# Optimization experiments

Hardware: AMD Instinct MI355X
Metric: run time of the kernel (lower is better)

The kernel has to match this reference:

```python
import jax, jax.numpy as jnp
import numpy as np

HID = 10
IN_DIM = 256
B, H, W = 8, 96, 96


def _conv(x, w, b=None, pad=0):
    y = jax.lax.conv_general_dilated(x, w, (1, 1), [(pad, pad), (pad, pad)],
                                     dimension_numbers=('NCHW', 'OIHW', 'NCHW'))
    return y if b is None else y + b[None, :, None, None]


def _bn(x, g, b):
    # eval-mode InPlaceABN(Sync) with identity running stats -> per-channel affine
    return x * g[None, :, None, None] + b[None, :, None, None]


def _branch(x, w1, g1, b1, w2, g2, b2):
    # Conv3x3 -> BN -> ReLU -> Conv1x1 -> BN -> ReLU  (relation / comp_u / comp_l)
    y = jax.nn.relu(_bn(_conv(x, w1, pad=1), g1, b1))
    return jax.nn.relu(_bn(_conv(y, w2), g2, b2))


def _gru(x, h, gw, gb, cw, cg, cb):
    # ConvGRU with 1x1 kernels
    gates = _conv(jnp.concatenate([x, h], axis=1), gw, gb)
    r = jax.nn.sigmoid(gates[:, 0:1])
    u = jax.nn.sigmoid(gates[:, 1:2])
    cnm = jax.nn.relu(_bn(_conv(jnp.concatenate([x, r * h], axis=1), cw), cg, cb))
    return (1.0 - u) * h + u * cnm


def setup_inputs():
    key = jax.random.key(0)
    ks = iter(jax.random.split(key, 48))

    def nrm(shape, s=0.05):
        return jax.random.normal(next(ks), shape, jnp.float32) * s

    inp = {
        'f_nodes': jax.random.normal(next(ks), (2, B, HID, H, W), jnp.float32),
        'h_nodes': jax.random.normal(next(ks), (3, B, HID, H, W), jnp.float32),
        'p_nodes': jax.random.normal(next(ks), (7, B, HID, H, W), jnp.float32),
        'xh': jax.random.normal(next(ks), (B, IN_DIM, H, W), jnp.float32),
        'f_atts': jax.random.uniform(next(ks), (2, B, 1, H, W), jnp.float32),
        'p_atts': jax.random.uniform(next(ks), (7, B, 1, H, W), jnp.float32),
        # Decomposition.decomp_att: Conv3x3(257->256)+BN+ReLU, Conv1x1(256->2)+bias
        'da_w1': nrm((IN_DIM, IN_DIM + 1, 3, 3)),
        'da_g1': jnp.ones((IN_DIM,), jnp.float32),
        'da_b1': jnp.zeros((IN_DIM,), jnp.float32),
        'da_w2': nrm((2, IN_DIM, 1, 1)),
        'da_b2': jnp.zeros((2,), jnp.float32),
    }
    # relation (shared across children), comp_u, comp_l: Conv3x3(20->10)+BN+ReLU, Conv1x1(10->10)+BN+ReLU
    for p in ('rel', 'cu', 'cl'):
        inp[p + '_w1'] = nrm((HID, 2 * HID, 3, 3))
        inp[p + '_g1'] = jnp.ones((HID,), jnp.float32)
        inp[p + '_b1'] = jnp.zeros((HID,), jnp.float32)
        inp[p + '_w2'] = nrm((HID, HID, 1, 1))
        inp[p + '_g2'] = jnp.ones((HID,), jnp.float32)
        inp[p + '_b2'] = jnp.zeros((HID,), jnp.float32)
    # 3 ConvGRUs (cls_h), 1x1 kernels, stacked on leading dim
    inp['gru_gw'] = nrm((3, 2, 2 * HID, 1, 1))
    inp['gru_gb'] = jnp.zeros((3, 2), jnp.float32)
    inp['gru_cw'] = nrm((3, HID, 2 * HID, 1, 1))
    inp['gru_cg'] = jnp.ones((3, HID), jnp.float32)
    inp['gru_cb'] = jnp.zeros((3, HID), jnp.float32)
    return inp


def reference(f_nodes, h_nodes, p_nodes, xh, f_atts, p_atts,
              da_w1, da_g1, da_b1, da_w2, da_b2,
              rel_w1, rel_g1, rel_b1, rel_w2, rel_g2, rel_b2,
              cu_w1, cu_g1, cu_b1, cu_w2, cu_g2, cu_b2,
              cl_w1, cl_g1, cl_b1, cl_w2, cl_g2, cl_b2,
              gru_gw, gru_gb, gru_cw, gru_cg, gru_cb):
    parent, parent_att = f_nodes[1], f_atts[1]
    # Decomposition of full-body node into 2 half nodes
    dm = _conv(jnp.concatenate([parent_att, xh], axis=1), da_w1, pad=1)
    dm = jax.nn.relu(_bn(dm, da_g1, da_b1))
    dm = _conv(dm, da_w2, da_b2)  # [B, 2, H, W] decomposition map
    datt = jax.nn.softmax(dm, axis=1)
    decomp = [_branch(jnp.concatenate([parent * datt[:, i:i + 1] * parent_att,
                                       h_nodes[1 + i]], axis=1),
                      rel_w1, rel_g1, rel_b1, rel_w2, rel_g2, rel_b2)
              for i in range(2)]
    # node 0: background
    n0 = _gru(f_nodes[0] + p_nodes[0], h_nodes[0],
              gru_gw[0], gru_gb[0], gru_cw[0], gru_cg[0], gru_cb[0])
    # node 1: upper half = composition(upper parts 1-4) + decomposition
    up = jnp.sum(p_nodes[1:5], axis=0) * jnp.sum(p_atts[1:5], axis=0)
    comp_u = _branch(jnp.concatenate([h_nodes[1], up], axis=1),
                     cu_w1, cu_g1, cu_b1, cu_w2, cu_g2, cu_b2)
    n1 = _gru(comp_u + decomp[0], h_nodes[1],
              gru_gw[1], gru_gb[1], gru_cw[1], gru_cg[1], gru_cb[1])
    # node 2: lower half = composition(lower parts 5-6) + decomposition
    lo = jnp.sum(p_nodes[5:7], axis=0) * jnp.sum(p_atts[5:7], axis=0)
    comp_l = _branch(jnp.concatenate([h_nodes[2], lo], axis=1),
                     cl_w1, cl_g1, cl_b1, cl_w2, cl_g2, cl_b2)
    n2 = _gru(comp_l + decomp[1], h_nodes[2],
              gru_gw[2], gru_gb[2], gru_cw[2], gru_cg[2], gru_cb[2])
    return (jnp.stack([n0, n1, n2]), dm)
```

## Files before the change

### kernel.cpp

```cpp
#include <hip/hip_runtime.h>
#include <cstddef>
#include <cstdint>

constexpr int Bn    = 8;
constexpr int Hn    = 96;
constexpr int Wn    = 96;
constexpr int HWn   = Hn * Wn;
constexpr int BHWn  = Bn * HWn;
constexpr int B10HW = Bn * 10 * HWn;

constexpr int XP_COLS        = 100;
constexpr int XP_ROWS        = 100;
constexpr int XP_PLANE       = XP_ROWS * XP_COLS;
constexpr int XP_PLANE_BYTES = XP_PLANE * 16;
constexpr int XP_OCT         = 36;

using short8  = __attribute__((ext_vector_type(8))) short;
using ushort8 = __attribute__((ext_vector_type(8))) unsigned short;
using float4v = __attribute__((ext_vector_type(4))) float;

__device__ __forceinline__ unsigned short f2bf(float f) {
    unsigned u = __builtin_bit_cast(unsigned, f);
    u += 0x7FFFu + ((u >> 16) & 1u);
    return (unsigned short)(u >> 16);
}

__device__ __forceinline__ void async16(const void* g, void* l) {
    auto gp = (__attribute__((address_space(1))) unsigned int*)(uintptr_t)g;
    auto lp = (__attribute__((address_space(3))) unsigned int*)(unsigned)(uintptr_t)l;
    __builtin_amdgcn_global_load_lds(gp, lp, 16, 0, 0);
}

struct BranchW  { const float *w1, *g1, *b1, *w2, *g2, *b2; };
struct BranchW3 { BranchW p[3]; };

constexpr int PACKW_BLOCKS = 2592;

__global__ void k_pack(const float* __restrict__ w1, short* __restrict__ wpk,
                       const float* __restrict__ xh, const float* __restrict__ patt,
                       ushort* __restrict__ xp)
{
    if (blockIdx.x < PACKW_BLOCKS) {
        const int o = blockIdx.x * 256 + threadIdx.x;
        const int j    = o & 7;
        const int lane = (o >> 3) & 63;
        const int q    = (o >> 9) & 15;
        const int t    = o >> 13;
        const int co   = q * 16 + (lane & 15);
        const int ci   = (t / 9) * 32 + ((lane >> 4) & 3) * 8 + j;
        const int tap  = t % 9;
        const float f  = (ci < 257) ? w1[((size_t)co * 257 + ci) * 9 + tap] : 0.f;
        wpk[o] = (short)f2bf(f);
    } else {
        const int g  = (blockIdx.x - PACKW_BLOCKS) * 256 + threadIdx.x;
        const int cw = g % XP_COLS;
        int t = g / XP_COLS;
        const int rh = t % XP_ROWS; t /= XP_ROWS;
        const int o  = t % XP_OCT;
        const int b  = t / XP_OCT;
        const int hh = rh - 1, ww = cw - 1;
        const bool inb = ((unsigned)hh < (unsigned)Hn) & ((unsigned)ww < (unsigned)Wn);
        const int off = hh * Wn + ww;
        ushort8 v;
        #pragma unroll
        for (int j = 0; j < 8; ++j) {
            const int ci = o * 8 + j;
            float f = 0.f;
            if (inb && ci < 257)
                f = (ci == 0) ? patt[b * HWn + off]
                              : xh[((size_t)b * 256 + (ci - 1)) * HWn + off];
            v[j] = f2bf(f);
        }
        *(ushort8*)&xp[(size_t)g * 8] = v;
    }
}

__global__ void k_packw(const float* __restrict__ w1, short* __restrict__ wpk)
{
    const int o = blockIdx.x * 256 + threadIdx.x;
    if (o >= 663552) return;
    const int j    = o & 7;
    const int lane = (o >> 3) & 63;
    const int q    = (o >> 9) & 15;
    const int t    = o >> 13;
    const int co   = q * 16 + (lane & 15);
    const int ci   = (t / 9) * 32 + ((lane >> 4) & 3) * 8 + j;
    const int tap  = t % 9;
    const float f  = (ci < 257) ? w1[((size_t)co * 257 + ci) * 9 + tap] : 0.f;
    wpk[o] = (short)f2bf(f);
}

__global__ __launch_bounds__(256, 3)
void k_bigconv3(const char* __restrict__ xp, const float* __restrict__ patt,
                const short* __restrict__ wpk, const float* __restrict__ g1,
                const float* __restrict__ b1, const float* __restrict__ w2,
                const float* __restrict__ db2,
                float* __restrict__ dm_out, float* __restrict__ s01)
{
    __shared__ __align__(16) short xs[3][4][194][8];
    __shared__ float part[4][64][2];

    const int tid  = threadIdx.x;
    const int lane = tid & 63;
    const int wid  = tid >> 6;
    const int bx   = blockIdx.x;
    const int b    = bx & 7;
    const int r2   = bx >> 3;
    const int wseg = r2 % 3;
    const int hb   = r2 / 3;
    const int h0   = hb * 2, w0 = wseg * 32;
    const int am   = lane & 15;
    const int aq   = lane >> 4;

    int poff[3];
    #pragma unroll
    for (int it = 0; it < 3; ++it) {
        const int pos = it * 64 + lane;
        const int row = pos / 34, col = pos - row * 34;
        poff[it] = ((h0 + row) * XP_COLS + (w0 + col)) * 16;
    }
    const char* xpb = xp + ((size_t)b * XP_OCT + wid) * XP_PLANE_BYTES;

    float4v acc[4][4];
    #pragma unroll
    for (int i = 0; i < 4; ++i)
        #pragma unroll
        for (int j = 0; j < 4; ++j)
            acc[i][j] = float4v{0.f, 0.f, 0.f, 0.f};

    int arow[4], acol[4];
    #pragma unroll
    for (int mt = 0; mt < 4; ++mt) {
        const int m = mt * 16 + am;
        arow[mt] = m >> 5;
        acol[mt] = m & 31;
    }

    auto stageX = [&](int cb, int buf) {
        const char* src = xpb + (size_t)cb * (4 * XP_PLANE_BYTES);
        #pragma unroll
        for (int it = 0; it < 3; ++it)
            async16(src + poff[it], &xs[buf][wid][it * 64][0]);
    };

    const short8* wp = (const short8*)wpk;
    const int qb = wid * 4;

    auto loadB = [&](int t, short8 (&dst)[4]) {
        #pragma unroll
        for (int nt = 0; nt < 4; ++nt)
            dst[nt] = wp[((size_t)t * 16 + qb + nt) * 64 + lane];
    };

    stageX(0, 0);
    stageX(1, 1);
    short8 bfr[3][4];
    loadB(0, bfr[0]);
    loadB(1, bfr[1]);

    for (int cb = 0; cb < 9; ++cb) {
        __builtin_amdgcn_sched_barrier(0);
        if (cb < 8) asm volatile("s_waitcnt vmcnt(3)" ::: "memory");
        else        asm volatile("s_waitcnt vmcnt(0)" ::: "memory");
        __builtin_amdgcn_s_barrier();
        __builtin_amdgcn_sched_barrier(0);
        if (cb < 7) stageX(cb + 2, (cb + 2) % 3);

        const int buf = cb % 3;
        #pragma unroll
        for (int tap = 0; tap < 9; ++tap) {
            const int t  = cb * 9 + tap;
            const int tl = (t + 2 <= 80) ? (t + 2) : 80;
            loadB(tl, bfr[(tap + 2) % 3]);
            const int kh = tap / 3, kw = tap % 3;
            short8 afr[4];
            #pragma unroll
            for (int mt = 0; mt < 4; ++mt) {
                const int pos = (arow[mt] + kh) * 34 + (acol[mt] + kw);
                afr[mt] = *(const short8*)&xs[buf][aq][pos][0];
            }
            __builtin_amdgcn_s_setprio(1);
            #pragma unroll
            for (int mt = 0; mt < 4; ++mt)
                #pragma unroll
                for (int nt = 0; nt < 4; ++nt)
                    acc[mt][nt] = __builtin_amdgcn_mfma_f32_16x16x32_bf16(
                        afr[mt], bfr[tap % 3][nt], acc[mt][nt], 0, 0, 0);
            __builtin_amdgcn_s_setprio(0);
        }
    }

    float gv[4], bv[4], wa[4], wbv[4];
    #pragma unroll
    for (int nt = 0; nt < 4; ++nt) {
        const int co = wid * 64 + nt * 16 + am;
        gv[nt]  = g1[co];
        bv[nt]  = b1[co];
        wa[nt]  = w2[co];
        wbv[nt] = w2[256 + co];
    }
    #pragma unroll
    for (int mt = 0; mt < 4; ++mt) {
        #pragma unroll
        for (int reg = 0; reg < 4; ++reg) {
            float s0 = 0.f, s1 = 0.f;
            #pragma unroll
            for (int nt = 0; nt < 4; ++nt) {
                const float y = fmaxf(fmaf(acc[mt][nt][reg], gv[nt], bv[nt]), 0.f);
                s0 = fmaf(wa[nt], y, s0);
                s1 = fmaf(wbv[nt], y, s1);
            }
            #pragma unroll
            for (int off = 1; off < 16; off <<= 1) {
                s0 += __shfl_xor(s0, off, 64);
                s1 += __shfl_xor(s1, off, 64);
            }
            if (am == 0) {
                const int m = mt * 16 + aq * 4 + reg;
                part[wid][m][0] = s0;
                part[wid][m][1] = s1;
            }
        }
    }
    __syncthreads();
    if (tid < 64) {
        const int m = tid, r = m >> 5, c = m & 31;
        const int off = (h0 + r) * Wn + (w0 + c);
        float d0 = part[0][m][0] + part[1][m][0] + part[2][m][0] + part[3][m][0] + db2[0];
        float d1 = part[0][m][1] + part[1][m][1] + part[2][m][1] + part[3][m][1] + db2[1];
        dm_out[(size_t)(b * 2) * HWn + off]     = d0;
        dm_out[(size_t)(b * 2 + 1) * HWn + off] = d1;
        const float mx = fmaxf(d0, d1);
        const float e0 = expf(d0 - mx), e1 = expf(d1 - mx);
        const float pa = patt[b * HWn + off];
        const float inv = pa / (e0 + e1);
        s01[b * HWn + off]        = e0 * inv;
        s01[BHWn + b * HWn + off] = e1 * inv;
    }
}

__global__ __launch_bounds__(256, 3)
void k_bigconv3_f(const float* __restrict__ xh, const float* __restrict__ patt,
                  const short* __restrict__ wpk, const float* __restrict__ g1,
                  const float* __restrict__ b1, const float* __restrict__ w2,
                  const float* __restrict__ db2,
                  float* __restrict__ dm_out, float* __restrict__ s01)
{
    __shared__ __align__(16) short xs[2][4][137][8];
    __shared__ float part[4][64][2];

    const int tid  = threadIdx.x;
    const int lane = tid & 63;
    const int wid  = tid >> 6;
    const int bx   = blockIdx.x;
    const int b    = bx & 7;
    const int r2   = bx >> 3;
    const int wseg = r2 % 3;
    const int hb   = r2 / 3;
    const int h0   = hb * 2, w0 = wseg * 32;
    const int am   = lane & 15;
    const int aq   = lane >> 4;

    float4v acc[4][4];
    #pragma unroll
    for (int i = 0; i < 4; ++i)
        #pragma unroll
        for (int j = 0; j < 4; ++j)
            acc[i][j] = float4v{0.f, 0.f, 0.f, 0.f};

    int arow[4], acol[4];
    #pragma unroll
    for (int mt = 0; mt < 4; ++mt) {
        const int m = mt * 16 + am;
        arow[mt] = m >> 5;
        acol[mt] = m & 31;
    }

    auto stageX = [&](int cb, int buf) {
        const int cig0 = cb * 32 + wid * 8;
        for (int pos = lane; pos < 136; pos += 64) {
            const int row = pos / 34, col = pos % 34;
            const int hh = h0 - 1 + row, ww = w0 - 1 + col;
            const bool inb = ((unsigned)hh < (unsigned)Hn) & ((unsigned)ww < (unsigned)Wn);
            const int off = hh * Wn + ww;
            ushort8 v;
            #pragma unroll
            for (int j = 0; j < 8; ++j) {
                const int ci = cig0 + j;
                float f = 0.f;
                if (inb && ci < 257)
                    f = (ci == 0) ? patt[b * HWn + off]
                                  : xh[((size_t)b * 256 + (ci - 1)) * HWn + off];
                v[j] = f2bf(f);
            }
            *(ushort8*)&xs[buf][wid][pos][0] = v;
        }
    };

    const short8* wp = (const short8*)wpk;
    const int qb = wid * 4;

    stageX(0, 0);
    short8 bfr[4], bnx[4];
    #pragma unroll
    for (int nt = 0; nt < 4; ++nt)
        bfr[nt] = wp[(size_t)(qb + nt) * 64 + lane];
    __syncthreads();

    for (int cb = 0; cb < 9; ++cb) {
        const int buf = cb & 1;
        for (int tap = 0; tap < 9; ++tap) {
            const int t = cb * 9 + tap;
            if (t < 80) {
                #pragma unroll
                for (int nt = 0; nt < 4; ++nt)
                    bnx[nt] = wp[((size_t)(t + 1) * 16 + qb + nt) * 64 + lane];
            }
            const int kh = tap / 3, kw = tap % 3;
            short8 afr[4];
            #pragma unroll
            for (int mt = 0; mt < 4; ++mt) {
                const int pos = (arow[mt] + kh) * 34 + (acol[mt] + kw);
                afr[mt] = *(const short8*)&xs[buf][aq][pos][0];
            }
            #pragma unroll
            for (int mt = 0; mt < 4; ++mt)
                #pragma unroll
                for (int nt = 0; nt < 4; ++nt)
                    acc[mt][nt] = __builtin_amdgcn_mfma_f32_16x16x32_bf16(
                        afr[mt], bfr[nt], acc[mt][nt], 0, 0, 0);
            #pragma unroll
            for (int nt = 0; nt < 4; ++nt) bfr[nt] = bnx[nt];
        }
        if (cb < 8) stageX(cb + 1, buf ^ 1);
        __syncthreads();
    }

    float gv[4], bv[4], wa[4], wbv[4];
    #pragma unroll
    for (int nt = 0; nt < 4; ++nt) {
        const int co = wid * 64 + nt * 16 + am;
        gv[nt]  = g1[co];
        bv[nt]  = b1[co];
        wa[nt]  = w2[co];
        wbv[nt] = w2[256 + co];
    }
    #pragma unroll
    for (int mt = 0; mt < 4; ++mt) {
        #pragma unroll
        for (int reg = 0; reg < 4; ++reg) {
            float s0 = 0.f, s1 = 0.f;
            #pragma unroll
            for (int nt = 0; nt < 4; ++nt) {
                const float y = fmaxf(fmaf(acc[mt][nt][reg], gv[nt], bv[nt]), 0.f);
                s0 = fmaf(wa[nt], y, s0);
                s1 = fmaf(wbv[nt], y, s1);
            }
            #pragma unroll
            for (int off = 1; off < 16; off <<= 1) {
                s0 += __shfl_xor(s0, off, 64);
                s1 += __shfl_xor(s1, off, 64);
            }
            if (am == 0) {
                const int m = mt * 16 + aq * 4 + reg;
                part[wid][m][0] = s0;
                part[wid][m][1] = s1;
            }
        }
    }
    __syncthreads();
    if (tid < 64) {
        const int m = tid, r = m >> 5, c = m & 31;
        const int off = (h0 + r) * Wn + (w0 + c);
        float d0 = part[0][m][0] + part[1][m][0] + part[2][m][0] + part[3][m][0] + db2[0];
        float d1 = part[0][m][1] + part[1][m][1] + part[2][m][1] + part[3][m][1] + db2[1];
        dm_out[(size_t)(b * 2) * HWn + off]     = d0;
        dm_out[(size_t)(b * 2 + 1) * HWn + off] = d1;
        const float mx = fmaxf(d0, d1);
        const float e0 = expf(d0 - mx), e1 = expf(d1 - mx);
        const float pa = patt[b * HWn + off];
        const float inv = pa / (e0 + e1);
        s01[b * HWn + off]        = e0 * inv;
        s01[BHWn + b * HWn + off] = e1 * inv;
    }
}

__global__ __launch_bounds__(256)
void k_branch(BranchW3 P, const float* __restrict__ parent, const float* __restrict__ h_nodes,
              const float* __restrict__ s01, const float* __restrict__ pn,
              const float* __restrict__ pa, float* __restrict__ bout)
{
    const int z  = blockIdx.y;
    const int pi = (z < 2) ? 0 : (z - 1);
    __shared__ float xt[20][10][34];
    __shared__ float paSum[340];
    __shared__ __align__(16) float wlt[9 * 20 * 12];
    __shared__ float w2l[100], g1l[10], b1l[10], g2l[10], b2l[10];

    const BranchW& Pw = P.p[pi];
    const int tid = threadIdx.x;
    for (int idx = tid; idx < 2160; idx += 256) {
        const int co = idx % 12, rem = idx / 12, ci = rem % 20, tap = rem / 20;
        wlt[idx] = (co < 10) ? Pw.w1[(co * 20 + ci) * 9 + tap] : 0.f;
    }
    if (tid < 100) w2l[tid] = Pw.w2[tid];
    if (tid < 10) {
        g1l[tid] = Pw.g1[tid]; b1l[tid] = Pw.b1[tid];
        g2l[tid] = Pw.g2[tid]; b2l[tid] = Pw.b2[tid];
    }

    const int bx = blockIdx.x;
    const int tw = bx % 3, th = (bx / 3) % 12, b = bx / 36;
    const int h0 = th * 8, w0 = tw * 32;

    const float* Ab;
    const float* sc = nullptr;
    const float* Bb = nullptr;
    int k0 = 0, k1 = -1;
    if (z == 0)      { Ab = parent; sc = s01;        Bb = h_nodes + (size_t)1 * B10HW; }
    else if (z == 1) { Ab = parent; sc = s01 + BHWn; Bb = h_nodes + (size_t)2 * B10HW; }
    else if (z == 2) { Ab = h_nodes + (size_t)1 * B10HW; k0 = 1; k1 = 4; }
    else             { Ab = h_nodes + (size_t)2 * B10HW; k0 = 5; k1 = 6; }

    if (z >= 2) {
        for (int idx = tid; idx < 340; idx += 256) {
            const int col = idx % 34, row = idx / 34;
            const int hh = h0 - 1 + row, ww = w0 - 1 + col;
            float s = 0.f;
            if (((unsigned)hh < (unsigned)Hn) & ((unsigned)ww < (unsigned)Wn)) {
                const int off = hh * Wn + ww;
                for (int k = k0; k <= k1; ++k)
                    s += pa[(size_t)(k * Bn + b) * HWn + off];
            }
            paSum[idx] = s;
        }
    }
    __syncthreads();

    for (int idx = tid; idx < 6800; idx += 256) {
        const int col = idx % 34, rem = idx / 34, row = rem % 10, ch = rem / 10;
        const int hh = h0 - 1 + row, ww = w0 - 1 + col;
        float v = 0.f;
        if (((unsigned)hh < (unsigned)Hn) & ((unsigned)ww < (unsigned)Wn)) {
            const int off = hh * Wn + ww;
            if (ch < 10) {
                v = Ab[((size_t)b * 10 + ch) * HWn + off];
                if (sc) v *= sc[b * HWn + off];
            } else if (z < 2) {
                v = Bb[((size_t)b * 10 + (ch - 10)) * HWn + off];
            } else {
                float s = 0.f;
                for (int k = k0; k <= k1; ++k)
                    s += pn[((size_t)(k * Bn + b) * 10 + (ch - 10)) * HWn + off];
                v = s * paSum[row * 34 + col];
            }
        }
        ((float*)xt)[idx] = v;
    }
    __syncthreads();

    const int r = tid >> 5, c = tid & 31;
    float a0 = 0, a1 = 0, a2 = 0, a3 = 0, a4 = 0, a5 = 0, a6 = 0, a7 = 0, a8 = 0, a9 = 0;
    #pragma unroll
    for (int tap = 0; tap < 9; ++tap) {
        const int kh = tap / 3, kw = tap % 3;
        #pragma unroll
        for (int ci = 0; ci < 20; ++ci) {
            const float xv = xt[ci][r + kh][c + kw];
            const float4 wA = *(const float4*)&wlt[(tap * 20 + ci) * 12];
            const float4 wB = *(const float4*)&wlt[(tap * 20 + ci) * 12 + 4];
            const float2 wC = *(const float2*)&wlt[(tap * 20 + ci) * 12 + 8];
            a0 = fmaf(wA.x, xv, a0); a1 = fmaf(wA.y, xv, a1);
            a2 = fmaf(wA.z, xv, a2); a3 = fmaf(wA.w, xv, a3);
            a4 = fmaf(wB.x, xv, a4); a5 = fmaf(wB.y, xv, a5);
            a6 = fmaf(wB.z, xv, a6); a7 = fmaf(wB.w, xv, a7);
            a8 = fmaf(wC.x, xv, a8); a9 = fmaf(wC.y, xv, a9);
        }
    }
    float acc[10] = {a0, a1, a2, a3, a4, a5, a6, a7, a8, a9};
    float y[10];
    #pragma unroll
    for (int co = 0; co < 10; ++co)
        y[co] = fmaxf(fmaf(acc[co], g1l[co], b1l[co]), 0.f);
    const int hw = (h0 + r) * Wn + (w0 + c);
    #pragma unroll
    for (int co = 0; co < 10; ++co) {
        float s = 0.f;
        #pragma unroll
        for (int i = 0; i < 10; ++i) s = fmaf(w2l[co * 10 + i], y[i], s);
        s = fmaxf(fmaf(s, g2l[co], b2l[co]), 0.f);
        bout[(size_t)z * B10HW + ((size_t)b * 10 + co) * HWn + hw] = s;
    }
}

__global__ void k_gru(const float* __restrict__ f_nodes, const float* __restrict__ h_nodes,
                      const float* __restrict__ p_nodes, const float* __restrict__ bout,
                      const float* __restrict__ gw, const float* __restrict__ gb,
                      const float* __restrict__ cw, const float* __restrict__ cg,
                      const float* __restrict__ cb, float* __restrict__ out)
{
    const int z = blockIdx.y;
    __shared__ float gwl[40], cwl[200], gbl[2], cgl[10], cbl[10];
    if (threadIdx.x < 40)  gwl[threadIdx.x] = gw[z * 40 + threadIdx.x];
    if (threadIdx.x < 200) cwl[threadIdx.x] = cw[z * 200 + threadIdx.x];
    if (threadIdx.x < 2)   gbl[threadIdx.x] = gb[z * 2 + threadIdx.x];
    if (threadIdx.x < 10) {
        cgl[threadIdx.x] = cg[z * 10 + threadIdx.x];
        cbl[threadIdx.x] = cb[z * 10 + threadIdx.x];
    }
    __syncthreads();

    const int p = blockIdx.x * 256 + threadIdx.x;
    const int b = p / HWn, hw = p % HWn;
    float x[10], h[10];
    #pragma unroll
    for (int c = 0; c < 10; ++c) {
        const size_t idx = ((size_t)b * 10 + c) * HWn + hw;
        if (z == 0)      x[c] = f_nodes[idx] + p_nodes[idx];
        else if (z == 1) x[c] = bout[(size_t)2 * B10HW + idx] + bout[idx];
        else             x[c] = bout[(size_t)3 * B10HW + idx] + bout[(size_t)1 * B10HW + idx];
        h[c] = h_nodes[(size_t)z * B10HW + idx];
    }
    float g0 = gbl[0], g1 = gbl[1];
    #pragma unroll
    for (int c = 0; c < 10; ++c) {
        g0 = fmaf(gwl[c],      x[c], g0);
        g0 = fmaf(gwl[10 + c], h[c], g0);
        g1 = fmaf(gwl[20 + c], x[c], g1);
        g1 = fmaf(gwl[30 + c], h[c], g1);
    }
    const float r = 1.f / (1.f + expf(-g0));
    const float u = 1.f / (1.f + expf(-g1));
    #pragma unroll
    for (int o = 0; o < 10; ++o) {
        float s = 0.f;
        #pragma unroll
        for (int c = 0; c < 10; ++c) {
            s = fmaf(cwl[o * 20 + c],      x[c],     s);
            s = fmaf(cwl[o * 20 + 10 + c], r * h[c], s);
        }
        s = fmaxf(fmaf(s, cgl[o], cbl[o]), 0.f);
        out[(size_t)z * B10HW + ((size_t)b * 10 + o) * HWn + hw] =
            (1.f - u) * h[o] + u * s;
    }
}

extern "C" void kernel_launch(void* const* d_in, const int* in_sizes, int n_in,
                              void* d_out, int out_size, void* d_ws, size_t ws_size,
                              hipStream_t stream)
{
    (void)in_sizes; (void)n_in; (void)out_size;

    const float* f_nodes = (const float*)d_in[0];
    const float* h_nodes = (const float*)d_in[1];
    const float* p_nodes = (const float*)d_in[2];
    const float* xh      = (const float*)d_in[3];
    const float* f_atts  = (const float*)d_in[4];
    const float* p_atts  = (const float*)d_in[5];
    const float* da_w1   = (const float*)d_in[6];
    const float* da_g1   = (const float*)d_in[7];
    const float* da_b1   = (const float*)d_in[8];
    const float* da_w2   = (const float*)d_in[9];
    const float* da_b2   = (const float*)d_in[10];

    BranchW3 P;
    for (int i = 0; i < 3; ++i) {
        P.p[i].w1 = (const float*)d_in[11 + 6 * i + 0];
        P.p[i].g1 = (const float*)d_in[11 + 6 * i + 1];
        P.p[i].b1 = (const float*)d_in[11 + 6 * i + 2];
        P.p[i].w2 = (const float*)d_in[11 + 6 * i + 3];
        P.p[i].g2 = (const float*)d_in[11 + 6 * i + 4];
        P.p[i].b2 = (const float*)d_in[11 + 6 * i + 5];
    }
    const float* gru_gw = (const float*)d_in[29];
    const float* gru_gb = (const float*)d_in[30];
    const float* gru_cw = (const float*)d_in[31];
    const float* gru_cg = (const float*)d_in[32];
    const float* gru_cb = (const float*)d_in[33];

    float* out    = (float*)d_out;
    float* dm_out = out + (size_t)3 * B10HW;

    float* ws   = (float*)d_ws;
    float* s01  = ws;
    float* bout = s01 + 2 * BHWn;
    short* wpk  = (short*)bout;
    const size_t XP_OFF_B = ((size_t)(2 * BHWn) + 4 * (size_t)B10HW) * 4;
    char*  xp   = (char*)d_ws + XP_OFF_B;
    const size_t WS_NEED = XP_OFF_B + (size_t)Bn * XP_OCT * XP_PLANE_BYTES;
    const bool use_packed = ws_size >= WS_NEED;

    const float* patt   = f_atts + BHWn;
    const float* parent = f_nodes + B10HW;

    if (use_packed) {
        k_pack<<<dim3(PACKW_BLOCKS + 11250), 256, 0, stream>>>(da_w1, wpk, xh, patt,
                                                               (ushort*)xp);
        k_bigconv3<<<dim3(1152), 256, 0, stream>>>(xp, patt, wpk, da_g1, da_b1,
                                                   da_w2, da_b2, dm_out, s01);
    } else {
        k_packw<<<dim3(2592), 256, 0, stream>>>(da_w1, wpk);
        k_bigconv3_f<<<dim3(1152), 256, 0, stream>>>(xh, patt, wpk, da_g1, da_b1,
                                                     da_w2, da_b2, dm_out, s01);
    }
    k_branch<<<dim3(288, 4), 256, 0, stream>>>(P, parent, h_nodes, s01,
                                               p_nodes, p_atts, bout);
    k_gru<<<dim3(288, 3), 256, 0, stream>>>(f_nodes, h_nodes, p_nodes, bout,
                                            gru_gw, gru_gb, gru_cw, gru_cg, gru_cb, out);
}
```

Before: 373.2 us.

## Fuse independent branch and GRU work into big-conv kernel launch

Merges the large 3x3 conv with the work that does not depend on its softmax output (the comp_u/comp_l branches and the background GRU node) into one kernel. Blocks are dispatched by index and share a union of shared-memory layouts. The remaining dependent branches and GRU nodes run in two follow-up kernels. The goal is to fill idle CUs during the conv tail and cut serialization between launches. The cost is that the union makes shared memory per block as large as its biggest member, and the fused kernel's register and occupancy profile may change.

```diff
diff --git a/kernel.cpp b/kernel.cpp
--- a/kernel.cpp
+++ b/kernel.cpp
@@ -33,6 +33,16 @@
 
 struct BranchW  { const float *w1, *g1, *b1, *w2, *g2, *b2; };
 struct BranchW3 { BranchW p[3]; };
+
+struct ConvSmem   { short xs[3][4][194][8]; float part[4][64][2]; };
+struct BranchSmem {
+    float xt[20][10][34];
+    float paSum[340];
+    float wlt[9 * 20 * 12];
+    float w2l[100], g1l[10], b1l[10], g2l[10], b2l[10];
+};
+struct GruSmem    { float gwl[40], cwl[200], gbl[2], cgl[10], cbl[10]; };
+union FusedSmem { ConvSmem c; BranchSmem b; GruSmem g; };
 
 constexpr int PACKW_BLOCKS = 2592;
 
@@ -90,326 +100,24 @@
     wpk[o] = (short)f2bf(f);
 }
 
-__global__ __launch_bounds__(256, 3)
-void k_bigconv3(const char* __restrict__ xp, const float* __restrict__ patt,
-                const short* __restrict__ wpk, const float* __restrict__ g1,
-                const float* __restrict__ b1, const float* __restrict__ w2,
-                const float* __restrict__ db2,
-                float* __restrict__ dm_out, float* __restrict__ s01)
-{
-    __shared__ __align__(16) short xs[3][4][194][8];
-    __shared__ float part[4][64][2];
-
-    const int tid  = threadIdx.x;
-    const int lane = tid & 63;
-    const int wid  = tid >> 6;
-    const int bx   = blockIdx.x;
-    const int b    = bx & 7;
-    const int r2   = bx >> 3;
-    const int wseg = r2 % 3;
-    const int hb   = r2 / 3;
-    const int h0   = hb * 2, w0 = wseg * 32;
-    const int am   = lane & 15;
-    const int aq   = lane >> 4;
-
-    int poff[3];
-    #pragma unroll
-    for (int it = 0; it < 3; ++it) {
-        const int pos = it * 64 + lane;
-        const int row = pos / 34, col = pos - row * 34;
-        poff[it] = ((h0 + row) * XP_COLS + (w0 + col)) * 16;
-    }
-    const char* xpb = xp + ((size_t)b * XP_OCT + wid) * XP_PLANE_BYTES;
-
-    float4v acc[4][4];
-    #pragma unroll
-    for (int i = 0; i < 4; ++i)
-        #pragma unroll
-        for (int j = 0; j < 4; ++j)
-            acc[i][j] = float4v{0.f, 0.f, 0.f, 0.f};
-
-    int arow[4], acol[4];
-    #pragma unroll
-    for (int mt = 0; mt < 4; ++mt) {
-        const int m = mt * 16 + am;
-        arow[mt] = m >> 5;
-        acol[mt] = m & 31;
-    }
-
-    auto stageX = [&](int cb, int buf) {
-        const char* src = xpb + (size_t)cb * (4 * XP_PLANE_BYTES);
-        #pragma unroll
-        for (int it = 0; it < 3; ++it)
-            async16(src + poff[it], &xs[buf][wid][it * 64][0]);
-    };
-
-    const short8* wp = (const short8*)wpk;
-    const int qb = wid * 4;
-
-    auto loadB = [&](int t, short8 (&dst)[4]) {
-        #pragma unroll
-        for (int nt = 0; nt < 4; ++nt)
-            dst[nt] = wp[((size_t)t * 16 + qb + nt) * 64 + lane];
-    };
-
-    stageX(0, 0);
-    stageX(1, 1);
-    short8 bfr[3][4];
-    loadB(0, bfr[0]);
-    loadB(1, bfr[1]);
-
-    for (int cb = 0; cb < 9; ++cb) {
-        __builtin_amdgcn_sched_barrier(0);
-        if (cb < 8) asm volatile("s_waitcnt vmcnt(3)" ::: "memory");
-        else        asm volatile("s_waitcnt vmcnt(0)" ::: "memory");
-        __builtin_amdgcn_s_barrier();
-        __builtin_amdgcn_sched_barrier(0);
-        if (cb < 7) stageX(cb + 2, (cb + 2) % 3);
-
-        const int buf = cb % 3;
-        #pragma unroll
-        for (int tap = 0; tap < 9; ++tap) {
-            const int t  = cb * 9 + tap;
-            const int tl = (t + 2 <= 80) ? (t + 2) : 80;
-            loadB(tl, bfr[(tap + 2) % 3]);
-            const int kh = tap / 3, kw = tap % 3;
-            short8 afr[4];
-            #pragma unroll
-            for (int mt = 0; mt < 4; ++mt) {
-                const int pos = (arow[mt] + kh) * 34 + (acol[mt] + kw);
-                afr[mt] = *(const short8*)&xs[buf][aq][pos][0];
-            }
-            __builtin_amdgcn_s_setprio(1);
-            #pragma unroll
-            for (int mt = 0; mt < 4; ++mt)
-                #pragma unroll
-                for (int nt = 0; nt < 4; ++nt)
-                    acc[mt][nt] = __builtin_amdgcn_mfma_f32_16x16x32_bf16(
-                        afr[mt], bfr[tap % 3][nt], acc[mt][nt], 0, 0, 0);
-            __builtin_amdgcn_s_setprio(0);
-        }
-    }
-
-    float gv[4], bv[4], wa[4], wbv[4];
-    #pragma unroll
-    for (int nt = 0; nt < 4; ++nt) {
-        const int co = wid * 64 + nt * 16 + am;
-        gv[nt]  = g1[co];
-        bv[nt]  = b1[co];
-        wa[nt]  = w2[co];
-        wbv[nt] = w2[256 + co];
-    }
-    #pragma unroll
-    for (int mt = 0; mt < 4; ++mt) {
-        #pragma unroll
-        for (int reg = 0; reg < 4; ++reg) {
-            float s0 = 0.f, s1 = 0.f;
-            #pragma unroll
-            for (int nt = 0; nt < 4; ++nt) {
-                const float y = fmaxf(fmaf(acc[mt][nt][reg], gv[nt], bv[nt]), 0.f);
-                s0 = fmaf(wa[nt], y, s0);
-                s1 = fmaf(wbv[nt], y, s1);
-            }
-            #pragma unroll
-            for (int off = 1; off < 16; off <<= 1) {
-                s0 += __shfl_xor(s0, off, 64);
-                s1 += __shfl_xor(s1, off, 64);
-            }
-            if (am == 0) {
-                const int m = mt * 16 + aq * 4 + reg;
-                part[wid][m][0] = s0;
-                part[wid][m][1] = s1;
-            }
-        }
-    }
-    __syncthreads();
-    if (tid < 64) {
-        const int m = tid, r = m >> 5, c = m & 31;
-        const int off = (h0 + r) * Wn + (w0 + c);
-        float d0 = part[0][m][0] + part[1][m][0] + part[2][m][0] + part[3][m][0] + db2[0];
-        float d1 = part[0][m][1] + part[1][m][1] + part[2][m][1] + part[3][m][1] + db2[1];
-        dm_out[(size_t)(b * 2) * HWn + off]     = d0;
-        dm_out[(size_t)(b * 2 + 1) * HWn + off] = d1;
-        const float mx = fmaxf(d0, d1);
-        const float e0 = expf(d0 - mx), e1 = expf(d1 - mx);
-        const float pa = patt[b * HWn + off];
-        const float inv = pa / (e0 + e1);
-        s01[b * HWn + off]        = e0 * inv;
-        s01[BHWn + b * HWn + off] = e1 * inv;
-    }
-}
-
-__global__ __launch_bounds__(256, 3)
-void k_bigconv3_f(const float* __restrict__ xh, const float* __restrict__ patt,
-                  const short* __restrict__ wpk, const float* __restrict__ g1,
-                  const float* __restrict__ b1, const float* __restrict__ w2,
-                  const float* __restrict__ db2,
-                  float* __restrict__ dm_out, float* __restrict__ s01)
-{
-    __shared__ __align__(16) short xs[2][4][137][8];
-    __shared__ float part[4][64][2];
-
-    const int tid  = threadIdx.x;
-    const int lane = tid & 63;
-    const int wid  = tid >> 6;
-    const int bx   = blockIdx.x;
-    const int b    = bx & 7;
-    const int r2   = bx >> 3;
-    const int wseg = r2 % 3;
-    const int hb   = r2 / 3;
-    const int h0   = hb * 2, w0 = wseg * 32;
-    const int am   = lane & 15;
-    const int aq   = lane >> 4;
-
-    float4v acc[4][4];
-    #pragma unroll
-    for (int i = 0; i < 4; ++i)
-        #pragma unroll
-        for (int j = 0; j < 4; ++j)
-            acc[i][j] = float4v{0.f, 0.f, 0.f, 0.f};
-
-    int arow[4], acol[4];
-    #pragma unroll
-    for (int mt = 0; mt < 4; ++mt) {
-        const int m = mt * 16 + am;
-        arow[mt] = m >> 5;
-        acol[mt] = m & 31;
-    }
-
-    auto stageX = [&](int cb, int buf) {
-        const int cig0 = cb * 32 + wid * 8;
-        for (int pos = lane; pos < 136; pos += 64) {
-            const int row = pos / 34, col = pos % 34;
-            const int hh = h0 - 1 + row, ww = w0 - 1 + col;
-            const bool inb = ((unsigned)hh < (unsigned)Hn) & ((unsigned)ww < (unsigned)Wn);
-            const int off = hh * Wn + ww;
-            ushort8 v;
-            #pragma unroll
-            for (int j = 0; j < 8; ++j) {
-                const int ci = cig0 + j;
-                float f = 0.f;
-                if (inb && ci < 257)
-                    f = (ci == 0) ? patt[b * HWn + off]
-                                  : xh[((size_t)b * 256 + (ci - 1)) * HWn + off];
-                v[j] = f2bf(f);
-            }
-            *(ushort8*)&xs[buf][wid][pos][0] = v;
-        }
-    };
-
-    const short8* wp = (const short8*)wpk;
-    const int qb = wid * 4;
-
-    stageX(0, 0);
-    short8 bfr[4], bnx[4];
-    #pragma unroll
-    for (int nt = 0; nt < 4; ++nt)
-        bfr[nt] = wp[(size_t)(qb + nt) * 64 + lane];
-    __syncthreads();
-
-    for (int cb = 0; cb < 9; ++cb) {
-        const int buf = cb & 1;
-        for (int tap = 0; tap < 9; ++tap) {
-            const int t = cb * 9 + tap;
-            if (t < 80) {
-                #pragma unroll
-                for (int nt = 0; nt < 4; ++nt)
-                    bnx[nt] = wp[((size_t)(t + 1) * 16 + qb + nt) * 64 + lane];
-            }
-            const int kh = tap / 3, kw = tap % 3;
-            short8 afr[4];
-            #pragma unroll
-            for (int mt = 0; mt < 4; ++mt) {
-                const int pos = (arow[mt] + kh) * 34 + (acol[mt] + kw);
-                afr[mt] = *(const short8*)&xs[buf][aq][pos][0];
-            }
-            #pragma unroll
-            for (int mt = 0; mt < 4; ++mt)
-                #pragma unroll
-                for (int nt = 0; nt < 4; ++nt)
-                    acc[mt][nt] = __builtin_amdgcn_mfma_f32_16x16x32_bf16(
-                        afr[mt], bfr[nt], acc[mt][nt], 0, 0, 0);
-            #pragma unroll
-            for (int nt = 0; nt < 4; ++nt) bfr[nt] = bnx[nt];
-        }
-        if (cb < 8) stageX(cb + 1, buf ^ 1);
-        __syncthreads();
-    }
-
-    float gv[4], bv[4], wa[4], wbv[4];
-    #pragma unroll
-    for (int nt = 0; nt < 4; ++nt) {
-        const int co = wid * 64 + nt * 16 + am;
-        gv[nt]  = g1[co];
-        bv[nt]  = b1[co];
-        wa[nt]  = w2[co];
-        wbv[nt] = w2[256 + co];
-    }
-    #pragma unroll
-    for (int mt = 0; mt < 4; ++mt) {
-        #pragma unroll
-        for (int reg = 0; reg < 4; ++reg) {
-            float s0 = 0.f, s1 = 0.f;
-            #pragma unroll
-            for (int nt = 0; nt < 4; ++nt) {
-                const float y = fmaxf(fmaf(acc[mt][nt][reg], gv[nt], bv[nt]), 0.f);
-                s0 = fmaf(wa[nt], y, s0);
-                s1 = fmaf(wbv[nt], y, s1);
-            }
-            #pragma unroll
-            for (int off = 1; off < 16; off <<= 1) {
-                s0 += __shfl_xor(s0, off, 64);
-                s1 += __shfl_xor(s1, off, 64);
-            }
-            if (am == 0) {
-                const int m = mt * 16 + aq * 4 + reg;
-                part[wid][m][0] = s0;
-                part[wid][m][1] = s1;
-            }
-        }
-    }
-    __syncthreads();
-    if (tid < 64) {
-        const int m = tid, r = m >> 5, c = m & 31;
-        const int off = (h0 + r) * Wn + (w0 + c);
-        float d0 = part[0][m][0] + part[1][m][0] + part[2][m][0] + part[3][m][0] + db2[0];
-        float d1 = part[0][m][1] + part[1][m][1] + part[2][m][1] + part[3][m][1] + db2[1];
-        dm_out[(size_t)(b * 2) * HWn + off]     = d0;
-        dm_out[(size_t)(b * 2 + 1) * HWn + off] = d1;
-        const float mx = fmaxf(d0, d1);
-        const float e0 = expf(d0 - mx), e1 = expf(d1 - mx);
-        const float pa = patt[b * HWn + off];
-        const float inv = pa / (e0 + e1);
-        s01[b * HWn + off]        = e0 * inv;
-        s01[BHWn + b * HWn + off] = e1 * inv;
-    }
-}
-
-__global__ __launch_bounds__(256)
-void k_branch(BranchW3 P, const float* __restrict__ parent, const float* __restrict__ h_nodes,
-              const float* __restrict__ s01, const float* __restrict__ pn,
-              const float* __restrict__ pa, float* __restrict__ bout)
-{
-    const int z  = blockIdx.y;
+__device__ __forceinline__ void branch_body(
+    BranchSmem& S, int z, int bx, int tid, const BranchW3& P,
+    const float* __restrict__ parent, const float* __restrict__ h_nodes,
+    const float* __restrict__ s01, const float* __restrict__ pn,
+    const float* __restrict__ pa, float* __restrict__ bout)
+{
     const int pi = (z < 2) ? 0 : (z - 1);
-    __shared__ float xt[20][10][34];
-    __shared__ float paSum[340];
-    __shared__ __align__(16) float wlt[9 * 20 * 12];
-    __shared__ float w2l[100], g1l[10], b1l[10], g2l[10], b2l[10];
-
     const BranchW& Pw = P.p[pi];
-    const int tid = threadIdx.x;
     for (int idx = tid; idx < 2160; idx += 256) {
         const int co = idx % 12, rem = idx / 12, ci = rem % 20, tap = rem / 20;
-        wlt[idx] = (co < 10) ? Pw.w1[(co * 20 + ci) * 9 + tap] : 0.f;
-    }
-    if (tid < 100) w2l[tid] = Pw.w2[tid];
+        S.wlt[idx] = (co < 10) ? Pw.w1[(co * 20 + ci) * 9 + tap] : 0.f;
+    }
+    if (tid < 100) S.w2l[tid] = Pw.w2[tid];
     if (tid < 10) {
-        g1l[tid] = Pw.g1[tid]; b1l[tid] = Pw.b1[tid];
-        g2l[tid] = Pw.g2[tid]; b2l[tid] = Pw.b2[tid];
-    }
-
-    const int bx = blockIdx.x;
+        S.g1l[tid] = Pw.g1[tid]; S.b1l[tid] = Pw.b1[tid];
+        S.g2l[tid] = Pw.g2[tid]; S.b2l[tid] = Pw.b2[tid];
+    }
+
     const int tw = bx % 3, th = (bx / 3) % 12, b = bx / 36;
     const int h0 = th * 8, w0 = tw * 32;
 
@@ -432,7 +140,7 @@
                 for (int k = k0; k <= k1; ++k)
                     s += pa[(size_t)(k * Bn + b) * HWn + off];
             }
-            paSum[idx] = s;
+            S.paSum[idx] = s;
         }
     }
     __syncthreads();
@@ -452,10 +160,10 @@
                 float s = 0.f;
                 for (int k = k0; k <= k1; ++k)
                     s += pn[((size_t)(k * Bn + b) * 10 + (ch - 10)) * HWn + off];
-                v = s * paSum[row * 34 + col];
-            }
-        }
-        ((float*)xt)[idx] = v;
+                v = s * S.paSum[row * 34 + col];
+            }
+        }
+        ((float*)S.xt)[idx] = v;
     }
     __syncthreads();
 
@@ -466,10 +174,10 @@
         const int kh = tap / 3, kw = tap % 3;
         #pragma unroll
         for (int ci = 0; ci < 20; ++ci) {
-            const float xv = xt[ci][r + kh][c + kw];
-            const float4 wA = *(const float4*)&wlt[(tap * 20 + ci) * 12];
-            const float4 wB = *(const float4*)&wlt[(tap * 20 + ci) * 12 + 4];
-            const float2 wC = *(const float2*)&wlt[(tap * 20 + ci) * 12 + 8];
+            const float xv = S.xt[ci][r + kh][c + kw];
+            const float4 wA = *(const float4*)&S.wlt[(tap * 20 + ci) * 12];
+            const float4 wB = *(const float4*)&S.wlt[(tap * 20 + ci) * 12 + 4];
+            const float2 wC = *(const float2*)&S.wlt[(tap * 20 + ci) * 12 + 8];
             a0 = fmaf(wA.x, xv, a0); a1 = fmaf(wA.y, xv, a1);
             a2 = fmaf(wA.z, xv, a2); a3 = fmaf(wA.w, xv, a3);
             a4 = fmaf(wB.x, xv, a4); a5 = fmaf(wB.y, xv, a5);
@@ -481,36 +189,36 @@
     float y[10];
     #pragma unroll
     for (int co = 0; co < 10; ++co)
-        y[co] = fmaxf(fmaf(acc[co], g1l[co], b1l[co]), 0.f);
+        y[co] = fmaxf(fmaf(acc[co], S.g1l[co], S.b1l[co]), 0.f);
     const int hw = (h0 + r) * Wn + (w0 + c);
     #pragma unroll
     for (int co = 0; co < 10; ++co) {
         float s = 0.f;
         #pragma unroll
-        for (int i = 0; i < 10; ++i) s = fmaf(w2l[co * 10 + i], y[i], s);
-        s = fmaxf(fmaf(s, g2l[co], b2l[co]), 0.f);
+        for (int i = 0; i < 10; ++i) s = fmaf(S.w2l[co * 10 + i], y[i], s);
+        s = fmaxf(fmaf(s, S.g2l[co], S.b2l[co]), 0.f);
         bout[(size_t)z * B10HW + ((size_t)b * 10 + co) * HWn + hw] = s;
     }
 }
 
-__global__ void k_gru(const float* __restrict__ f_nodes, const float* __restrict__ h_nodes,
-                      const float* __restrict__ p_nodes, const float* __restrict__ bout,
-                      const float* __restrict__ gw, const float* __restrict__ gb,
-                      const float* __restrict__ cw, const float* __restrict__ cg,
-                      const float* __restrict__ cb, float* __restrict__ out)
-{
-    const int z = blockIdx.y;
-    __shared__ float gwl[40], cwl[200], gbl[2], cgl[10], cbl[10];
-    if (threadIdx.x < 40)  gwl[threadIdx.x] = gw[z * 40 + threadIdx.x];
-    if (threadIdx.x < 200) cwl[threadIdx.x] = cw[z * 200 + threadIdx.x];
-    if (threadIdx.x < 2)   gbl[threadIdx.x] = gb[z * 2 + threadIdx.x];
-    if (threadIdx.x < 10) {
-        cgl[threadIdx.x] = cg[z * 10 + threadIdx.x];
-        cbl[threadIdx.x] = cb[z * 10 + threadIdx.x];
+__device__ __forceinline__ void gru_body(
+    GruSmem& S, int z, int bx, int tid,
+    const float* __restrict__ f_nodes, const float* __restrict__ h_nodes,
+    const float* __restrict__ p_nodes, const float* __restrict__ bout,
+    const float* __restrict__ gw, const float* __restrict__ gb,
+    const float* __restrict__ cw, const float* __restrict__ cg,
+    const float* __restrict__ cb, float* __restrict__ out)
+{
+    if (tid < 40)  S.gwl[tid] = gw[z * 40 + tid];
+    if (tid < 200) S.cwl[tid] = cw[z * 200 + tid];
+    if (tid < 2)   S.gbl[tid] = gb[z * 2 + tid];
+    if (tid < 10) {
+        S.cgl[tid] = cg[z * 10 + tid];
+        S.cbl[tid] = cb[z * 10 + tid];
     }
     __syncthreads();
 
-    const int p = blockIdx.x * 256 + threadIdx.x;
+    const int p = bx * 256 + tid;
     const int b = p / HWn, hw = p % HWn;
     float x[10], h[10];
     #pragma unroll
@@ -521,13 +229,13 @@
         else             x[c] = bout[(size_t)3 * B10HW + idx] + bout[(size_t)1 * B10HW + idx];
         h[c] = h_nodes[(size_t)z * B10HW + idx];
     }
-    float g0 = gbl[0], g1 = gbl[1];
+    float g0 = S.gbl[0], g1 = S.gbl[1];
     #pragma unroll
     for (int c = 0; c < 10; ++c) {
-        g0 = fmaf(gwl[c],      x[c], g0);
-        g0 = fmaf(gwl[10 + c], h[c], g0);
-        g1 = fmaf(gwl[20 + c], x[c], g1);
-        g1 = fmaf(gwl[30 + c], h[c], g1);
+        g0 = fmaf(S.gwl[c],      x[c], g0);
+        g0 = fmaf(S.gwl[10 + c], h[c], g0);
+        g1 = fmaf(S.gwl[20 + c], x[c], g1);
+        g1 = fmaf(S.gwl[30 + c], h[c], g1);
     }
     const float r = 1.f / (1.f + expf(-g0));
     const float u = 1.f / (1.f + expf(-g1));
@@ -536,12 +244,375 @@
         float s = 0.f;
         #pragma unroll
         for (int c = 0; c < 10; ++c) {
-            s = fmaf(cwl[o * 20 + c],      x[c],     s);
-            s = fmaf(cwl[o * 20 + 10 + c], r * h[c], s);
-        }
-        s = fmaxf(fmaf(s, cgl[o], cbl[o]), 0.f);
+            s = fmaf(S.cwl[o * 20 + c],      x[c],     s);
+            s = fmaf(S.cwl[o * 20 + 10 + c], r * h[c], s);
+        }
+        s = fmaxf(fmaf(s, S.cgl[o], S.cbl[o]), 0.f);
         out[(size_t)z * B10HW + ((size_t)b * 10 + o) * HWn + hw] =
             (1.f - u) * h[o] + u * s;
+    }
+}
+
+constexpr int CONV_BLOCKS = 1152;
+
+__global__ __launch_bounds__(256, 3)
+void k_fused(const char* __restrict__ xp, const float* __restrict__ patt,
+             const short* __restrict__ wpk, const float* __restrict__ g1,
+             const float* __restrict__ b1, const float* __restrict__ w2,
+             const float* __restrict__ db2,
+             float* __restrict__ dm_out, float* __restrict__ s01,
+             BranchW3 P, const float* __restrict__ parent,
+             const float* __restrict__ h_nodes, const float* __restrict__ pn,
+             const float* __restrict__ pa, float* __restrict__ bout,
+             const float* __restrict__ f_nodes, const float* __restrict__ p_nodes,
+             const float* __restrict__ gw, const float* __restrict__ gb,
+             const float* __restrict__ cw, const float* __restrict__ cg,
+             const float* __restrict__ cb, float* __restrict__ out)
+{
+    __shared__ __align__(16) FusedSmem sm;
+    const int tid = threadIdx.x;
+    const int bxg = blockIdx.x;
+
+    if (bxg >= CONV_BLOCKS) {
+        const int r = bxg - CONV_BLOCKS;
+        if (r < 576) {
+            const int z = (r < 288) ? 2 : 3;
+            branch_body(sm.b, z, (r < 288) ? r : r - 288, tid, P, parent,
+                        h_nodes, s01, pn, pa, bout);
+        } else {
+            gru_body(sm.g, 0, r - 576, tid, f_nodes, h_nodes, p_nodes, bout,
+                     gw, gb, cw, cg, cb, out);
+        }
+        return;
+    }
+
+    const int lane = tid & 63;
+    const int wid  = tid >> 6;
+    const int bx   = bxg;
+    const int b    = bx & 7;
+    const int r2   = bx >> 3;
+    const int wseg = r2 % 3;
+    const int hb   = r2 / 3;
+    const int h0   = hb * 2, w0 = wseg * 32;
+    const int am   = lane & 15;
+    const int aq   = lane >> 4;
+
+    int poff[3];
+    #pragma unroll
+    for (int it = 0; it < 3; ++it) {
+        const int pos = it * 64 + lane;
+        const int row = pos / 34, col = pos - row * 34;
+        poff[it] = ((h0 + row) * XP_COLS + (w0 + col)) * 16;
+    }
+    const char* xpb = xp + ((size_t)b * XP_OCT + wid) * XP_PLANE_BYTES;
+
+    float4v acc[4][4];
+    #pragma unroll
+    for (int i = 0; i < 4; ++i)
+        #pragma unroll
+        for (int j = 0; j < 4; ++j)
+            acc[i][j] = float4v{0.f, 0.f, 0.f, 0.f};
+
+    int arow[4], acol[4];
+    #pragma unroll
+    for (int mt = 0; mt < 4; ++mt) {
+        const int m = mt * 16 + am;
+        arow[mt] = m >> 5;
+        acol[mt] = m & 31;
+    }
+
+    auto stageX = [&](int cb, int buf) {
+        const char* src = xpb + (size_t)cb * (4 * XP_PLANE_BYTES);
+        #pragma unroll
+        for (int it = 0; it < 3; ++it)
+            async16(src + poff[it], &sm.c.xs[buf][wid][it * 64][0]);
+    };
+
+    const short8* wp = (const short8*)wpk;
+    const int qb = wid * 4;
+
+    auto loadB = [&](int t, short8 (&dst)[4]) {
+        #pragma unroll
+        for (int nt = 0; nt < 4; ++nt)
+            dst[nt] = wp[((size_t)t * 16 + qb + nt) * 64 + lane];
+    };
+
+    stageX(0, 0);
+    stageX(1, 1);
+    short8 bfr[3][4];
+    loadB(0, bfr[0]);
+    loadB(1, bfr[1]);
+
+    for (int cb = 0; cb < 9; ++cb) {
+        __builtin_amdgcn_sched_barrier(0);
+        if (cb < 8) asm volatile("s_waitcnt vmcnt(3)" ::: "memory");
+        else        asm volatile("s_waitcnt vmcnt(0)" ::: "memory");
+        __builtin_amdgcn_s_barrier();
+        __builtin_amdgcn_sched_barrier(0);
+        if (cb < 7) stageX(cb + 2, (cb + 2) % 3);
+
+        const int buf = cb % 3;
+        #pragma unroll
+        for (int tap = 0; tap < 9; ++tap) {
+            const int t  = cb * 9 + tap;
+            const int tl = (t + 2 <= 80) ? (t + 2) : 80;
+            loadB(tl, bfr[(tap + 2) % 3]);
+            const int kh = tap / 3, kw = tap % 3;
+            short8 afr[4];
+            #pragma unroll
+            for (int mt = 0; mt < 4; ++mt) {
+                const int pos = (arow[mt] + kh) * 34 + (acol[mt] + kw);
+                afr[mt] = *(const short8*)&sm.c.xs[buf][aq][pos][0];
+            }
+            __builtin_amdgcn_s_setprio(1);
+            #pragma unroll
+            for (int mt = 0; mt < 4; ++mt)
+                #pragma unroll
+                for (int nt = 0; nt < 4; ++nt)
+                    acc[mt][nt] = __builtin_amdgcn_mfma_f32_16x16x32_bf16(
+                        afr[mt], bfr[tap % 3][nt], acc[mt][nt], 0, 0, 0);
+            __builtin_amdgcn_s_setprio(0);
+        }
+    }
+
+    float gv[4], bv[4], wa[4], wbv[4];
+    #pragma unroll
+    for (int nt = 0; nt < 4; ++nt) {
+        const int co = wid * 64 + nt * 16 + am;
+        gv[nt]  = g1[co];
+        bv[nt]  = b1[co];
+        wa[nt]  = w2[co];
+        wbv[nt] = w2[256 + co];
+    }
+    #pragma unroll
+    for (int mt = 0; mt < 4; ++mt) {
+        #pragma unroll
+        for (int reg = 0; reg < 4; ++reg) {
+            float s0 = 0.f, s1 = 0.f;
+            #pragma unroll
+            for (int nt = 0; nt < 4; ++nt) {
+                const float y = fmaxf(fmaf(acc[mt][nt][reg], gv[nt], bv[nt]), 0.f);
+                s0 = fmaf(wa[nt], y, s0);
+                s1 = fmaf(wbv[nt], y, s1);
+            }
+            #pragma unroll
+            for (int off = 1; off < 16; off <<= 1) {
+                s0 += __shfl_xor(s0, off, 64);
+                s1 += __shfl_xor(s1, off, 64);
+            }
+            if (am == 0) {
+                const int m = mt * 16 + aq * 4 + reg;
+                sm.c.part[wid][m][0] = s0;
+                sm.c.part[wid][m][1] = s1;
+            }
+        }
+    }
+    __syncthreads();
+    if (tid < 64) {
+        const int m = tid, r = m >> 5, c = m & 31;
+        const int off = (h0 + r) * Wn + (w0 + c);
+        float d0 = sm.c.part[0][m][0] + sm.c.part[1][m][0] + sm.c.part[2][m][0]
+                 + sm.c.part[3][m][0] + db2[0];
+        float d1 = sm.c.part[0][m][1] + sm.c.part[1][m][1] + sm.c.part[2][m][1]
+                 + sm.c.part[3][m][1] + db2[1];
+        dm_out[(size_t)(b * 2) * HWn + off]     = d0;
+        dm_out[(size_t)(b * 2 + 1) * HWn + off] = d1;
+        const float mx = fmaxf(d0, d1);
+        const float e0 = expf(d0 - mx), e1 = expf(d1 - mx);
+        const float pa2 = patt[b * HWn + off];
+        const float inv = pa2 / (e0 + e1);
+        s01[b * HWn + off]        = e0 * inv;
+        s01[BHWn + b * HWn + off] = e1 * inv;
+    }
+}
+
+__global__ __launch_bounds__(256)
+void k_branch01(BranchW3 P, const float* __restrict__ parent,
+                const float* __restrict__ h_nodes, const float* __restrict__ s01,
+                const float* __restrict__ pn, const float* __restrict__ pa,
+                float* __restrict__ bout)
+{
+    __shared__ __align__(16) BranchSmem S;
+    branch_body(S, blockIdx.y, blockIdx.x, threadIdx.x, P, parent, h_nodes,
+                s01, pn, pa, bout);
+}
+
+__global__ void k_gru12(const float* __restrict__ f_nodes, const float* __restrict__ h_nodes,
+                        const float* __restrict__ p_nodes, const float* __restrict__ bout,
+                        const float* __restrict__ gw, const float* __restrict__ gb,
+                        const float* __restrict__ cw, const float* __restrict__ cg,
+                        const float* __restrict__ cb, float* __restrict__ out)
+{
+    __shared__ GruSmem S;
+    gru_body(S, blockIdx.y + 1, blockIdx.x, threadIdx.x, f_nodes, h_nodes,
+             p_nodes, bout, gw, gb, cw, cg, cb, out);
+}
+
+__global__ __launch_bounds__(256)
+void k_branch_all(BranchW3 P, const float* __restrict__ parent,
+                  const float* __restrict__ h_nodes, const float* __restrict__ s01,
+                  const float* __restrict__ pn, const float* __restrict__ pa,
+                  float* __restrict__ bout)
+{
+    __shared__ __align__(16) BranchSmem S;
+    branch_body(S, blockIdx.y, blockIdx.x, threadIdx.x, P, parent, h_nodes,
+                s01, pn, pa, bout);
+}
+
+__global__ void k_gru_all(const float* __restrict__ f_nodes, const float* __restrict__ h_nodes,
+                          const float* __restrict__ p_nodes, const float* __restrict__ bout,
+                          const float* __restrict__ gw, const float* __restrict__ gb,
+                          const float* __restrict__ cw, const float* __restrict__ cg,
+                          const float* __restrict__ cb, float* __restrict__ out)
+{
+    __shared__ GruSmem S;
+    gru_body(S, blockIdx.y, blockIdx.x, threadIdx.x, f_nodes, h_nodes,
+             p_nodes, bout, gw, gb, cw, cg, cb, out);
+}
+
+__global__ __launch_bounds__(256, 3)
+void k_bigconv3_f(const float* __restrict__ xh, const float* __restrict__ patt,
+                  const short* __restrict__ wpk, const float* __restrict__ g1,
+                  const float* __restrict__ b1, const float* __restrict__ w2,
+                  const float* __restrict__ db2,
+                  float* __restrict__ dm_out, float* __restrict__ s01)
+{
+    __shared__ __align__(16) short xs[2][4][137][8];
+    __shared__ float part[4][64][2];
+
+    const int tid  = threadIdx.x;
+    const int lane = tid & 63;
+    const int wid  = tid >> 6;
+    const int bx   = blockIdx.x;
+    const int b    = bx & 7;
+    const int r2   = bx >> 3;
+    const int wseg = r2 % 3;
+    const int hb   = r2 / 3;
+    const int h0   = hb * 2, w0 = wseg * 32;
+    const int am   = lane & 15;
+    const int aq   = lane >> 4;
+
+    float4v acc[4][4];
+    #pragma unroll
+    for (int i = 0; i < 4; ++i)
+        #pragma unroll
+        for (int j = 0; j < 4; ++j)
+            acc[i][j] = float4v{0.f, 0.f, 0.f, 0.f};
+
+    int arow[4], acol[4];
+    #pragma unroll
+    for (int mt = 0; mt < 4; ++mt) {
+        const int m = mt * 16 + am;
+        arow[mt] = m >> 5;
+        acol[mt] = m & 31;
+    }
+
+    auto stageX = [&](int cb, int buf) {
+        const int cig0 = cb * 32 + wid * 8;
+        for (int pos = lane; pos < 136; pos += 64) {
+            const int row = pos / 34, col = pos % 34;
+            const int hh = h0 - 1 + row, ww = w0 - 1 + col;
+            const bool inb = ((unsigned)hh < (unsigned)Hn) & ((unsigned)ww < (unsigned)Wn);
+            const int off = hh * Wn + ww;
+            ushort8 v;
+            #pragma unroll
+            for (int j = 0; j < 8; ++j) {
+                const int ci = cig0 + j;
+                float f = 0.f;
+                if (inb && ci < 257)
+                    f = (ci == 0) ? patt[b * HWn + off]
+                                  : xh[((size_t)b * 256 + (ci - 1)) * HWn + off];
+                v[j] = f2bf(f);
+            }
+            *(ushort8*)&xs[buf][wid][pos][0] = v;
+        }
+    };
+
+    const short8* wp = (const short8*)wpk;
+    const int qb = wid * 4;
+
+    stageX(0, 0);
+    short8 bfr[4], bnx[4];
+    #pragma unroll
+    for (int nt = 0; nt < 4; ++nt)
+        bfr[nt] = wp[(size_t)(qb + nt) * 64 + lane];
+    __syncthreads();
+
+    for (int cb = 0; cb < 9; ++cb) {
+        const int buf = cb & 1;
+        for (int tap = 0; tap < 9; ++tap) {
+            const int t = cb * 9 + tap;
+            if (t < 80) {
+                #pragma unroll
+                for (int nt = 0; nt < 4; ++nt)
+                    bnx[nt] = wp[((size_t)(t + 1) * 16 + qb + nt) * 64 + lane];
+            }
+            const int kh = tap / 3, kw = tap % 3;
+            short8 afr[4];
+            #pragma unroll
+            for (int mt = 0; mt < 4; ++mt) {
+                const int pos = (arow[mt] + kh) * 34 + (acol[mt] + kw);
+                afr[mt] = *(const short8*)&xs[buf][aq][pos][0];
+            }
+            #pragma unroll
+            for (int mt = 0; mt < 4; ++mt)
+                #pragma unroll
+                for (int nt = 0; nt < 4; ++nt)
+                    acc[mt][nt] = __builtin_amdgcn_mfma_f32_16x16x32_bf16(
+                        afr[mt], bfr[nt], acc[mt][nt], 0, 0, 0);
+            #pragma unroll
+            for (int nt = 0; nt < 4; ++nt) bfr[nt] = bnx[nt];
+        }
+        if (cb < 8) stageX(cb + 1, buf ^ 1);
+        __syncthreads();
+    }
+
+    float gv[4], bv[4], wa[4], wbv[4];
+    #pragma unroll
+    for (int nt = 0; nt < 4; ++nt) {
+        const int co = wid * 64 + nt * 16 + am;
+        gv[nt]  = g1[co];
+        bv[nt]  = b1[co];
+        wa[nt]  = w2[co];
+        wbv[nt] = w2[256 + co];
+    }
+    #pragma unroll
+    for (int mt = 0; mt < 4; ++mt) {
+        #pragma unroll
+        for (int reg = 0; reg < 4; ++reg) {
+            float s0 = 0.f, s1 = 0.f;
+            #pragma unroll
+            for (int nt = 0; nt < 4; ++nt) {
+                const float y = fmaxf(fmaf(acc[mt][nt][reg], gv[nt], bv[nt]), 0.f);
+                s0 = fmaf(wa[nt], y, s0);
+                s1 = fmaf(wbv[nt], y, s1);
+            }
+            #pragma unroll
+            for (int off = 1; off < 16; off <<= 1) {
+                s0 += __shfl_xor(s0, off, 64);
+                s1 += __shfl_xor(s1, off, 64);
+            }
+            if (am == 0) {
+                const int m = mt * 16 + aq * 4 + reg;
+                part[wid][m][0] = s0;
+                part[wid][m][1] = s1;
+            }
+        }
+    }
+    __syncthreads();
+    if (tid < 64) {
+        const int m = tid, r = m >> 5, c = m & 31;
+        const int off = (h0 + r) * Wn + (w0 + c);
+        float d0 = part[0][m][0] + part[1][m][0] + part[2][m][0] + part[3][m][0] + db2[0];
+        float d1 = part[0][m][1] + part[1][m][1] + part[2][m][1] + part[3][m][1] + db2[1];
+        dm_out[(size_t)(b * 2) * HWn + off]     = d0;
+        dm_out[(size_t)(b * 2 + 1) * HWn + off] = d1;
+        const float mx = fmaxf(d0, d1);
+        const float e0 = expf(d0 - mx), e1 = expf(d1 - mx);
+        const float pa = patt[b * HWn + off];
+        const float inv = pa / (e0 + e1);
+        s01[b * HWn + off]        = e0 * inv;
+        s01[BHWn + b * HWn + off] = e1 * inv;
     }
 }
 
@@ -596,15 +667,23 @@
     if (use_packed) {
         k_pack<<<dim3(PACKW_BLOCKS + 11250), 256, 0, stream>>>(da_w1, wpk, xh, patt,
                                                                (ushort*)xp);
-        k_bigconv3<<<dim3(1152), 256, 0, stream>>>(xp, patt, wpk, da_g1, da_b1,
-                                                   da_w2, da_b2, dm_out, s01);
+        k_fused<<<dim3(CONV_BLOCKS + 576 + 288), 256, 0, stream>>>(
+            xp, patt, wpk, da_g1, da_b1, da_w2, da_b2, dm_out, s01,
+            P, parent, h_nodes, p_nodes, p_atts, bout,
+            f_nodes, p_nodes, gru_gw, gru_gb, gru_cw, gru_cg, gru_cb, out);
+        k_branch01<<<dim3(288, 2), 256, 0, stream>>>(P, parent, h_nodes, s01,
+                                                     p_nodes, p_atts, bout);
+        k_gru12<<<dim3(288, 2), 256, 0, stream>>>(f_nodes, h_nodes, p_nodes, bout,
+                                                  gru_gw, gru_gb, gru_cw, gru_cg,
+                                                  gru_cb, out);
     } else {
         k_packw<<<dim3(2592), 256, 0, stream>>>(da_w1, wpk);
         k_bigconv3_f<<<dim3(1152), 256, 0, stream>>>(xh, patt, wpk, da_g1, da_b1,
                                                      da_w2, da_b2, dm_out, s01);
-    }
-    k_branch<<<dim3(288, 4), 256, 0, stream>>>(P, parent, h_nodes, s01,
-                                               p_nodes, p_atts, bout);
-    k_gru<<<dim3(288, 3), 256, 0, stream>>>(f_nodes, h_nodes, p_nodes, bout,
-                                            gru_gw, gru_gb, gru_cw, gru_cg, gru_cb, out);
-}
+        k_branch_all<<<dim3(288, 4), 256, 0, stream>>>(P, parent, h_nodes, s01,
+                                                       p_nodes, p_atts, bout);
+        k_gru_all<<<dim3(288, 3), 256, 0, stream>>>(f_nodes, h_nodes, p_nodes, bout,
+                                                    gru_gw, gru_gb, gru_cw, gru_cg,
+                                                    gru_cb, out);
+    }
+}
```

New measurement: 360.2 us (median of 3 runs). 3.5% less time.
